# Kernel tuning notes

Measured on AMD Instinct MI355X. Metric: run time of the kernel, lower is better.

The kernel has to match this reference:

```python
import jax, jax.numpy as jnp
import numpy as np

C = 8; E = 512; HEADS = 8; DH = E // HEADS; M = 256; PINV_ITERS = 6; KW = 33

def layer_norm(x, g, b):
    mu = x.mean(-1, keepdims=True)
    xm = x - mu
    v = (xm * xm).mean(-1, keepdims=True)
    return xm / jnp.sqrt(v + 1e-5) * g + b

def mp_pinv(x, iters=PINV_ITERS):
    # Moore-Penrose pseudoinverse via Newton-Schulz iterations (lucidrains nystrom-attention)
    I = jnp.eye(x.shape[-1], dtype=x.dtype)
    ax = jnp.abs(x)
    z = jnp.swapaxes(x, -1, -2) / (jnp.max(ax.sum(-2)) * jnp.max(ax.sum(-1)))
    for _ in range(iters):
        xz = x @ z
        z = 0.25 * z @ (13. * I - xz @ (15. * I - xz @ (7. * I - xz)))
    return z

def nystrom_attn(x, mask, Wqkv, Wout, bout, conv_w):
    b, n0, d = x.shape
    pad = (-n0) % M  # left-pad so seq divisible by num_landmarks
    x = jnp.pad(x, ((0, 0), (pad, 0), (0, 0)))
    mask = jnp.pad(mask, ((0, 0), (pad, 0)))
    n = n0 + pad
    qkv = (x @ Wqkv).reshape(b, n, 3, HEADS, DH).transpose(2, 0, 3, 1, 4)
    q, k, v = qkv[0], qkv[1], qkv[2]  # [b,h,n,dh]
    mf = mask[:, None, :, None].astype(x.dtype)
    q = q * mf * (DH ** -0.5); k = k * mf; v = v * mf
    l = n // M
    mls = mask.reshape(b, 1, M, l).sum(-1).astype(x.dtype)  # valid count per landmark segment
    div = mls[..., None] + 1e-8
    ql = q.reshape(b, HEADS, M, l, DH).sum(3) / div
    kl = k.reshape(b, HEADS, M, l, DH).sum(3) / div
    mland = mls > 0  # [b,1,M]
    neg = -jnp.finfo(x.dtype).max / 2
    sim1 = jnp.where(mask[:, None, :, None] & mland[..., None, :], jnp.einsum('bhid,bhjd->bhij', q, kl), neg)
    sim2 = jnp.where(mland[..., :, None] & mland[..., None, :], jnp.einsum('bhid,bhjd->bhij', ql, kl), neg)
    sim3 = jnp.where(mland[..., :, None] & mask[:, None, None, :], jnp.einsum('bhid,bhjd->bhij', ql, k), neg)
    a1 = jax.nn.softmax(sim1, -1); a2 = jax.nn.softmax(sim2, -1); a3 = jax.nn.softmax(sim3, -1)
    out = (a1 @ mp_pinv(a2)) @ (a3 @ v)
    # residual depthwise conv over sequence dim (residual=True in NystromAttention)
    out = out + jax.lax.conv_general_dilated(v, conv_w, (1, 1), ((KW // 2, KW // 2), (0, 0)),
                                             dimension_numbers=('NCHW', 'OIHW', 'NCHW'),
                                             feature_group_count=HEADS)
    out = out.transpose(0, 2, 1, 3).reshape(b, n, d) @ Wout + bout
    return out[:, pad:]

def _forward(h, W1, b1, cls_token, pmt_token, ln1_g, ln1_b, Wqkv1, Wout1, bout1, conv1,
             ln0_g, ln0_b, Wqkv0, Wout0, bout0, conv0, lnf_g, lnf_b, W3, b3):
    N = h.shape[0]
    h1 = jax.nn.relu(h @ W1 + b1)  # _fc1
    seq = jnp.concatenate([cls_token, pmt_token, h1], 0)[None]  # [1, 1+C+N, E]
    y = nystrom_attn(layer_norm(seq, ln1_g, ln1_b), jnp.ones((1, seq.shape[1]), bool),
                     Wqkv1, Wout1, bout1, conv1)
    x = seq + y  # layer1 (TransLayer_custom)
    pmt = x[:, 1:1 + C, :]   # new pmt tokens [1,C,E]
    toks = x[:, 1 + C:, :]   # [1,N,E]
    assn = jax.nn.softmax(jnp.einsum('bnd,bcd->bnc', toks, pmt), -1)
    idx = jnp.argmax(assn[0], -1)  # [N] cluster assignment
    # cluster dispatch: per-cluster [pmt_i; tokens-of-cluster-i] run of shared layer0, via masking
    xs = jnp.concatenate([pmt[0][:, None, :], jnp.broadcast_to(toks[0], (C, N, E))], 1)  # [C,1+N,E]
    masks = jnp.concatenate([jnp.ones((C, 1), bool), idx[None, :] == jnp.arange(C)[:, None]], 1)
    def trans0(xi, mi):
        xi = xi[None]
        return (xi + nystrom_attn(layer_norm(xi, ln0_g, ln0_b), mi[None], Wqkv0, Wout0, bout0, conv0))[0]
    out = jax.vmap(trans0)(xs, masks)  # [C,1+N,E]
    h_un = out[:, 1:, :][idx, jnp.arange(N)]  # each token from its own cluster's run
    order = jnp.argsort(idx)  # stable: groups tokens by cluster, preserving order (concat order)
    h_global = h_un[order]; idx_new = idx[order]
    hcat = jnp.concatenate([x[0, 0][None], h_global], 0)  # [1+N, E]
    hn = layer_norm(hcat, lnf_g, lnf_b)
    sums = jax.ops.segment_sum(hcat[1:], idx_new, num_segments=C)
    counts = jax.ops.segment_sum(jnp.ones((N,), h.dtype), idx_new, num_segments=C)
    merge = sums / jnp.maximum(counts, 1.)[:, None]  # CTM merge token per cluster
    ptc = jnp.linalg.norm(pmt[0] @ pmt[0].T - jnp.eye(C, dtype=h.dtype))
    tok_out = jnp.concatenate([hn[0][None], merge], 0).mean(0)
    logit = tok_out @ W3 + b3
    return logit, ptc

def setup_inputs() -> dict:
    key = jax.random.key(0)
    ks = jax.random.split(key, 16)
    N, IN_DIM, NC = 4096, 1024, 2
    s = 0.02
    q, _ = jnp.linalg.qr(jax.random.normal(ks[15], (E, C)))  # orthonormal pmt init
    return {
        'h': jax.random.normal(ks[0], (N, IN_DIM)),
        'W1': jax.random.normal(ks[1], (IN_DIM, E)) * s, 'b1': jnp.zeros((E,)),
        'cls_token': jax.random.normal(ks[2], (1, E)),
        'pmt_token': q.T,
        'ln1_g': jnp.ones((E,)), 'ln1_b': jnp.zeros((E,)),
        'Wqkv1': jax.random.normal(ks[3], (E, 3 * E)) * s,
        'Wout1': jax.random.normal(ks[4], (E, E)) * s, 'bout1': jnp.zeros((E,)),
        'conv1': jax.random.normal(ks[5], (HEADS, 1, KW, 1)) * s,
        'ln0_g': jnp.ones((E,)), 'ln0_b': jnp.zeros((E,)),
        'Wqkv0': jax.random.normal(ks[6], (E, 3 * E)) * s,
        'Wout0': jax.random.normal(ks[7], (E, E)) * s, 'bout0': jnp.zeros((E,)),
        'conv0': jax.random.normal(ks[8], (HEADS, 1, KW, 1)) * s,
        'lnf_g': jnp.ones((E,)), 'lnf_b': jnp.zeros((E,)),
        'W3': jax.random.normal(ks[9], (E, NC)) * s, 'b3': jnp.zeros((NC,)),
    }

def reference(h, W1, b1, cls_token, pmt_token, ln1_g, ln1_b, Wqkv1, Wout1, bout1, conv1,
              ln0_g, ln0_b, Wqkv0, Wout0, bout0, conv0, lnf_g, lnf_b, W3, b3):
    logit, ptc = _forward(h, W1, b1, cls_token, pmt_token, ln1_g, ln1_b, Wqkv1, Wout1, bout1, conv1,
                          ln0_g, ln0_b, Wqkv0, Wout0, bout0, conv0, lnf_g, lnf_b, W3, b3)
    return (logit[None], jax.nn.softmax(logit)[None], ptc)
```

## Files before the change

### kernel.cpp

```cpp
#include <hip/hip_runtime.h>

#define NEGV (-1.70141173e38f)

constexpr int E    = 512;
constexpr int NTOK = 4096;
constexpr int NPAD = 4352;
constexpr int PAD1 = 247;
constexpr int NSEQ = 4105;
constexpr int NG   = 5120;
constexpr int NTP  = 4104;

typedef __attribute__((ext_vector_type(8))) short short8;
typedef __attribute__((ext_vector_type(4))) float float4v;

__device__ inline float bf2f(ushort u){ return __uint_as_float(((unsigned)u)<<16); }
__device__ inline ushort f2bf(float f){
  unsigned u = __float_as_uint(f);
  unsigned r = (u + 0x7FFFu + ((u>>16)&1u)) >> 16;
  return (ushort)r;
}
__device__ inline short8 pack8u(const ushort* u) {
  union { short8 v; unsigned w[4]; } x;
  x.w[0] = (unsigned)u[0] | ((unsigned)u[1] << 16);
  x.w[1] = (unsigned)u[2] | ((unsigned)u[3] << 16);
  x.w[2] = (unsigned)u[4] | ((unsigned)u[5] << 16);
  x.w[3] = (unsigned)u[6] | ((unsigned)u[7] << 16);
  return x.v;
}

template<int BT, bool BOUNDS>
__global__ __launch_bounds__(256) void k_mm(
    const ushort* __restrict__ A, const ushort* __restrict__ B,
    const float* __restrict__ bias, const float* __restrict__ resid,
    float* __restrict__ Cf, ushort* __restrict__ Cb,
    int M, int N, int K, int ksplit, int ldC,
    long sA, long sB, long sC,
    const int* __restrict__ colsel, const int* __restrict__ rowsel,
    int zmodA, int zmodB, const int* __restrict__ krange, int kshift,
    float alpha, float bdiag, int flags)
{
  const int z = blockIdx.z;
  const int batch = z / ksplit, ks = z - batch * ksplit;
  const int kslice = K / ksplit;
  int kbeg = ks * kslice, kend = kbeg + kslice;
  if (krange) { int ki = batch >> kshift; kbeg = krange[2*ki]; kend = krange[2*ki+1]; }
  long aoff;
  if (colsel) { int s = colsel[blockIdx.x]; if (s < 0) s = 0; aoff = (long)(s*8 + batch) * sA; }
  else aoff = (long)(zmodA ? (batch & (zmodA-1)) : batch) * sA;
  long boff;
  if (rowsel) { int s = rowsel[blockIdx.y]; if (s < 0) s = 0; boff = (long)(s*8 + batch) * sB; }
  else boff = (long)(zmodB ? (batch & (zmodB-1)) : batch) * sB;
  A += aoff; B += boff;
  const long coff = (long)z * sC;

  __shared__ __align__(16) ushort Al[4][128][8];
  __shared__ __align__(16) ushort Bl[4][128][8];

  const int tid  = threadIdx.x;
  const int lane = tid & 63, wid = tid >> 6;
  const int wr = wid >> 1, wc = wid & 1;
  const int l4 = lane >> 4, l15 = lane & 15;
  const int row0 = blockIdx.y * 128, col0 = blockIdx.x * 128;

  float4v acc[4][4];
#pragma unroll
  for (int i = 0; i < 4; ++i)
#pragma unroll
    for (int j = 0; j < 4; ++j) acc[i][j] = (float4v){0.f,0.f,0.f,0.f};

  for (int k0 = kbeg; k0 < kend; k0 += 32) {
    __syncthreads();
#pragma unroll
    for (int e = 0; e < 2; ++e) {
      int id = tid * 2 + e; int m = id >> 2, kb = id & 3;
      uint4 v = make_uint4(0u,0u,0u,0u);
      int gr = row0 + m;
      if (!BOUNDS || gr < M)
        v = *reinterpret_cast<const uint4*>(A + (long)gr * K + k0 + kb * 8);
      *reinterpret_cast<uint4*>(&Al[kb][m][0]) = v;
    }
    if (BT) {
#pragma unroll
      for (int e = 0; e < 2; ++e) {
        int id = tid * 2 + e; int n = id >> 2, kb = id & 3;
        uint4 v = make_uint4(0u,0u,0u,0u);
        int gc = col0 + n;
        if (!BOUNDS || gc < N)
          v = *reinterpret_cast<const uint4*>(B + (long)gc * K + k0 + kb * 8);
        *reinterpret_cast<uint4*>(&Bl[kb][n][0]) = v;
      }
    } else {
      int n = tid & 127, gc = col0 + n;
      bool inb = (!BOUNDS || gc < N);
#pragma unroll
      for (int e = 0; e < 2; ++e) {
        int kb = (tid >> 7) * 2 + e;
        ushort u[8];
#pragma unroll
        for (int j = 0; j < 8; ++j) {
          int gk = k0 + kb * 8 + j;
          ushort val = inb ? B[(long)gk * N + gc] : (ushort)0;
          if (flags & 4) {
            float f = bdiag * (gk == gc ? 1.f : 0.f) - bf2f(val);
            val = f2bf(f);
          }
          u[j] = val;
        }
        uint4 w;
        w.x = (unsigned)u[0] | ((unsigned)u[1] << 16);
        w.y = (unsigned)u[2] | ((unsigned)u[3] << 16);
        w.z = (unsigned)u[4] | ((unsigned)u[5] << 16);
        w.w = (unsigned)u[6] | ((unsigned)u[7] << 16);
        *reinterpret_cast<uint4*>(&Bl[kb][n][0]) = w;
      }
    }
    __syncthreads();
    short8 af[4], bg[4];
#pragma unroll
    for (int mi = 0; mi < 4; ++mi)
      af[mi] = *reinterpret_cast<const short8*>(&Al[l4][wr*64 + mi*16 + l15][0]);
#pragma unroll
    for (int ni = 0; ni < 4; ++ni)
      bg[ni] = *reinterpret_cast<const short8*>(&Bl[l4][wc*64 + ni*16 + l15][0]);
#pragma unroll
    for (int mi = 0; mi < 4; ++mi)
#pragma unroll
      for (int ni = 0; ni < 4; ++ni)
        acc[mi][ni] = __builtin_amdgcn_mfma_f32_16x16x32_bf16(af[mi], bg[ni], acc[mi][ni], 0, 0, 0);
  }
#pragma unroll
  for (int mi = 0; mi < 4; ++mi)
#pragma unroll
    for (int ni = 0; ni < 4; ++ni)
#pragma unroll
      for (int r = 0; r < 4; ++r) {
        int row = row0 + wr*64 + mi*16 + l4*4 + r;
        int col = col0 + wc*64 + ni*16 + l15;
        if (BOUNDS && (row >= M || col >= N)) continue;
        float v = alpha * acc[mi][ni][r];
        if (flags & 1) v += bias[col];
        if (flags & 2) v = fmaxf(v, 0.f);
        if (flags & 8) v += resid[(long)row * ldC + col];
        long off = coff + (long)row * ldC + col;
        if (flags & 16) Cb[off] = f2bf(v); else Cf[off] = v;
      }
}

static void mm(hipStream_t st, const void* A, const void* B, const float* bias, const float* resid,
               float* Cf, ushort* Cb, int M, int N, int K, int nb, int ksplit, int ldC,
               long sA, long sB, long sC,
               const int* colsel, const int* rowsel, int zmodA, int zmodB,
               const int* krange, int kshift,
               float alpha, float bdiag, int flags, bool bt, bool bounds)
{
  dim3 g((N + 127) / 128, (M + 127) / 128, nb * ksplit), b(256);
  const ushort* a = (const ushort*)A; const ushort* bb = (const ushort*)B;
  if (bt) {
    if (bounds) k_mm<1, true ><<<g, b, 0, st>>>(a, bb, bias, resid, Cf, Cb, M, N, K, ksplit, ldC, sA, sB, sC, colsel, rowsel, zmodA, zmodB, krange, kshift, alpha, bdiag, flags);
    else        k_mm<1, false><<<g, b, 0, st>>>(a, bb, bias, resid, Cf, Cb, M, N, K, ksplit, ldC, sA, sB, sC, colsel, rowsel, zmodA, zmodB, krange, kshift, alpha, bdiag, flags);
  } else {
    if (bounds) k_mm<0, true ><<<g, b, 0, st>>>(a, bb, bias, resid, Cf, Cb, M, N, K, ksplit, ldC, sA, sB, sC, colsel, rowsel, zmodA, zmodB, krange, kshift, alpha, bdiag, flags);
    else        k_mm<0, false><<<g, b, 0, st>>>(a, bb, bias, resid, Cf, Cb, M, N, K, ksplit, ldC, sA, sB, sC, colsel, rowsel, zmodA, zmodB, krange, kshift, alpha, bdiag, flags);
  }
}

__device__ __forceinline__ void gsync() {
  __threadfence();
  __syncthreads();
}

template<int AMODE, int BMODE>
__device__ __forceinline__ void wg_gemm256(
    const ushort* __restrict__ Ag, const ushort* __restrict__ Bg,
    ushort (* __restrict__ Yl)[256], ushort (* __restrict__ Btl)[256],
    float4v acc[8][4], int tid)
{
  const int lane = tid & 63;
  const int wid  = tid >> 6;
  const int wr = wid >> 2, wc = wid & 3;
  const int l4 = lane >> 4, l15 = lane & 15;
#pragma unroll 1
  for (int kt = 0; kt < 8; ++kt) {
    const int k0 = kt * 32;
    if (BMODE == 0) {
      __syncthreads();
      int kk = tid >> 4, n0 = (tid & 15) * 16;
      int s = (kk >> 3) << 4;
      const ushort* src = Bg + (long)(k0 + kk) * 256 + n0;
      *reinterpret_cast<uint4*>(&Btl[kk][n0 ^ s])       = *reinterpret_cast<const uint4*>(src);
      *reinterpret_cast<uint4*>(&Btl[kk][(n0 + 8) ^ s]) = *reinterpret_cast<const uint4*>(src + 8);
      __syncthreads();
    }
    short8 af[8];
#pragma unroll
    for (int mi = 0; mi < 8; ++mi) {
      int r = wr * 128 + mi * 16 + l15;
      if (AMODE == 0) {
        af[mi] = *reinterpret_cast<const short8*>(Ag + (long)r * 256 + k0 + l4 * 8);
      } else {
        int sr = ((r >> 3) & 3) << 4;
        af[mi] = *reinterpret_cast<const short8*>(&Yl[r][(k0 + l4 * 8) ^ sr]);
      }
    }
    short8 bf[4];
#pragma unroll
    for (int ni = 0; ni < 4; ++ni) {
      int c = wc * 64 + ni * 16 + l15;
      ushort u[8];
      if (BMODE == 0) {
        int kb = l4 * 8;
        int cc = c ^ ((kb >> 3) << 4);
#pragma unroll
        for (int j = 0; j < 8; ++j) u[j] = Btl[kb + j][cc];
      } else {
        int kb = k0 + l4 * 8;
        int cc = c ^ (((kb >> 3) & 3) << 4);
#pragma unroll
        for (int j = 0; j < 8; ++j) u[j] = Yl[kb + j][cc];
      }
      bf[ni] = pack8u(u);
    }
#pragma unroll
    for (int mi = 0; mi < 8; ++mi)
#pragma unroll
      for (int ni = 0; ni < 4; ++ni)
        acc[mi][ni] = __builtin_amdgcn_mfma_f32_16x16x32_bf16(af[mi], bf[ni], acc[mi][ni], 0, 0, 0);
  }
}

__global__ __launch_bounds__(512) void k_pinv_chain(
    const ushort* __restrict__ Xall, ushort* __restrict__ ZAall, ushort* __restrict__ ZBall,
    ushort* __restrict__ T1all, ushort* __restrict__ T2all, const float* __restrict__ sc)
{
  __shared__ ushort Yl[256][256];
  __shared__ ushort Btl[32][256];
  const int bt = blockIdx.x;
  const ushort* X = Xall + (long)bt * 65536;
  ushort* Z0 = ZAall + (long)bt * 65536;
  ushort* Z1 = ZBall + (long)bt * 65536;
  ushort* T1 = T1all + (long)bt * 65536;
  ushort* T2 = T2all + (long)bt * 65536;
  const int tid = threadIdx.x;
  const int lane = tid & 63, wid = tid >> 6;
  const int wr = wid >> 2, wc = wid & 3;
  const int l4 = lane >> 4, l15 = lane & 15;
  const float scale = sc[bt >> 3];

  {
    int r = tid & 255, half = tid >> 8;
    for (int c0 = half * 128; c0 < half * 128 + 128; c0 += 8) {
      ushort u[8];
#pragma unroll
      for (int j = 0; j < 8; ++j)
        u[j] = f2bf(bf2f(X[(long)(c0 + j) * 256 + r]) * scale);
      *reinterpret_cast<short8*>(Z0 + (long)r * 256 + c0) = pack8u(u);
    }
  }
  gsync();

  ushort* Zc = Z0;
  ushort* Zn = Z1;
  float4v acc[8][4];

  for (int it = 0; it < 6; ++it) {
#pragma unroll
    for (int i = 0; i < 8; ++i)
#pragma unroll
      for (int j = 0; j < 4; ++j) acc[i][j] = (float4v){0.f,0.f,0.f,0.f};
    wg_gemm256<0,0>(X, Zc, Yl, Btl, acc, tid);
    __syncthreads();
#pragma unroll
    for (int mi = 0; mi < 8; ++mi)
#pragma unroll
      for (int ni = 0; ni < 4; ++ni)
#pragma unroll
        for (int ri = 0; ri < 4; ++ri) {
          int row = wr*128 + mi*16 + l4*4 + ri;
          int col = wc*64 + ni*16 + l15;
          Yl[row][col ^ (((row >> 3) & 3) << 4)] = f2bf(acc[mi][ni][ri]);
        }
    __syncthreads();
#pragma unroll
    for (int i = 0; i < 8; ++i)
#pragma unroll
      for (int j = 0; j < 4; ++j) acc[i][j] = (float4v){0.f,0.f,0.f,0.f};
    wg_gemm256<1,1>(nullptr, nullptr, Yl, Btl, acc, tid);
#pragma unroll
    for (int mi = 0; mi < 8; ++mi)
#pragma unroll
      for (int ni = 0; ni < 4; ++ni)
#pragma unroll
        for (int ri = 0; ri < 4; ++ri) {
          int row = wr*128 + mi*16 + l4*4 + ri;
          int col = wc*64 + ni*16 + l15;
          float y = bf2f(Yl[row][col ^ (((row >> 3) & 3) << 4)]);
          T1[(long)row*256 + col] = f2bf(7.f*y - acc[mi][ni][ri]);
        }
    gsync();
#pragma unroll
    for (int i = 0; i < 8; ++i)
#pragma unroll
      for (int j = 0; j < 4; ++j) acc[i][j] = (float4v){0.f,0.f,0.f,0.f};
    wg_gemm256<1,0>(nullptr, T1, Yl, Btl, acc, tid);
#pragma unroll
    for (int mi = 0; mi < 8; ++mi)
#pragma unroll
      for (int ni = 0; ni < 4; ++ni)
#pragma unroll
        for (int ri = 0; ri < 4; ++ri) {
          int row = wr*128 + mi*16 + l4*4 + ri;
          int col = wc*64 + ni*16 + l15;
          float y = bf2f(Yl[row][col ^ (((row >> 3) & 3) << 4)]);
          T2[(long)row*256 + col] = f2bf(15.f*y - acc[mi][ni][ri]);
        }
    gsync();
#pragma unroll
    for (int i = 0; i < 8; ++i)
#pragma unroll
      for (int j = 0; j < 4; ++j) acc[i][j] = (float4v){0.f,0.f,0.f,0.f};
    wg_gemm256<0,0>(Zc, T2, Yl, Btl, acc, tid);
#pragma unroll
    for (int mi = 0; mi < 8; ++mi)
#pragma unroll
      for (int ni = 0; ni < 4; ++ni)
#pragma unroll
        for (int ri = 0; ri < 4; ++ri) {
          int row = wr*128 + mi*16 + l4*4 + ri;
          int col = wc*64 + ni*16 + l15;
          float zv = bf2f(Zc[(long)row*256 + col]);
          Zn[(long)row*256 + col] = f2bf(0.25f*(13.f*zv - acc[mi][ni][ri]));
        }
    gsync();
    ushort* tmp = Zc; Zc = Zn; Zn = tmp;
  }
}

__global__ __launch_bounds__(256) void k_colmax(const ushort* __restrict__ X, float* __restrict__ sc) {
  int cl = blockIdx.x, j = threadIdx.x;
  float cmax = 0.f;
  for (int h = 0; h < 8; ++h) {
    const ushort* mat = X + (long)(cl * 8 + h) * 65536;
    float cs = 0.f;
    for (int i = 0; i < 256; ++i) cs += bf2f(mat[i * 256 + j]);
    cmax = fmaxf(cmax, cs);
  }
  __shared__ float red[256];
  red[j] = cmax; __syncthreads();
  for (int o = 128; o > 0; o >>= 1) { if (j < o) red[j] = fmaxf(red[j], red[j + o]); __syncthreads(); }
  if (j == 0) sc[cl] = 1.f / red[0];
}

__global__ void k_prep0(const float* __restrict__ cls, const float* __restrict__ pmt, float* __restrict__ seq) {
  int i = blockIdx.x * 256 + threadIdx.x;
  if (i < 512) seq[i] = cls[i];
  else if (i < 4608) seq[i] = pmt[i - 512];
}
__global__ void k_cvt(const float* __restrict__ s, ushort* __restrict__ d, long n) {
  long i = (long)blockIdx.x * 256 + threadIdx.x;
  if (i < n) d[i] = f2bf(s[i]);
}
__global__ void k_tcvt_all(const float* __restrict__ W1, const float* __restrict__ Wq1,
                           const float* __restrict__ Wq0, const float* __restrict__ Wo1,
                           const float* __restrict__ Wo0,
                           ushort* __restrict__ W1t, ushort* __restrict__ Wq1t,
                           ushort* __restrict__ Wq0t, ushort* __restrict__ Wo1t,
                           ushort* __restrict__ Wo0t) {
  const float* W; ushort* Wt; int K, N;
  switch (blockIdx.z) {
    case 0:  W = W1;  Wt = W1t;  K = 1024; N = 512;  break;
    case 1:  W = Wq1; Wt = Wq1t; K = 512;  N = 1536; break;
    case 2:  W = Wq0; Wt = Wq0t; K = 512;  N = 1536; break;
    case 3:  W = Wo1; Wt = Wo1t; K = 512;  N = 512;  break;
    default: W = Wo0; Wt = Wo0t; K = 512;  N = 512;  break;
  }
  int nb_ = blockIdx.x * 32, kb = blockIdx.y * 32;
  if (nb_ >= N || kb >= K) return;
  __shared__ float tile[32][33];
  int tx = threadIdx.x, ty = threadIdx.y;
  for (int r = ty; r < 32; r += 8) tile[r][tx] = W[(long)(kb + r) * N + nb_ + tx];
  __syncthreads();
  for (int r = ty; r < 32; r += 8) Wt[(long)(nb_ + r) * K + kb + tx] = f2bf(tile[tx][r]);
}

__device__ __forceinline__ void ln_row(const float* __restrict__ xr, const float* __restrict__ g,
                                       const float* __restrict__ b, ushort* __restrict__ yr,
                                       float* red, int t) {
  float v0 = xr[t], v1 = xr[t + 256];
  red[t] = v0 + v1; __syncthreads();
  for (int o = 128; o > 0; o >>= 1) { if (t < o) red[t] += red[t + o]; __syncthreads(); }
  float mu = red[0] * (1.f / E); __syncthreads();
  float d0 = v0 - mu, d1 = v1 - mu;
  red[t] = d0 * d0 + d1 * d1; __syncthreads();
  for (int o = 128; o > 0; o >>= 1) { if (t < o) red[t] += red[t + o]; __syncthreads(); }
  float inv = 1.f / sqrtf(red[0] * (1.f / E) + 1e-5f);
  yr[t]       = f2bf(d0 * inv * g[t]       + b[t]);
  yr[t + 256] = f2bf(d1 * inv * g[t + 256] + b[t + 256]);
}

__global__ __launch_bounds__(256) void k_lnB(const float* __restrict__ x, const float* __restrict__ g,
                                             const float* __restrict__ b, ushort* __restrict__ y) {
  int row = blockIdx.x, t = threadIdx.x;
  ushort* yr = y + (long)row * E;
  if (row < PAD1) { yr[t] = 0; yr[t + 256] = 0; return; }
  __shared__ float red[256];
  ln_row(x + (long)(row - PAD1) * E, g, b, yr, red, t);
}
__global__ __launch_bounds__(256) void k_lnC(const float* __restrict__ seq, const float* __restrict__ g,
                                             const float* __restrict__ b, ushort* __restrict__ y) {
  int row = blockIdx.x, t = threadIdx.x;
  const float* xr = (row < 8) ? (seq + 512 + (long)row * E) : (seq + 9 * 512 + (long)(row - 8) * E);
  __shared__ float red[256];
  ln_row(xr, g, b, y + (long)row * E, red, t);
}

__global__ void k_buildQKVB(const float* __restrict__ qkv, ushort* __restrict__ Qb,
                            ushort* __restrict__ Kb, ushort* __restrict__ Vt) {
  int h = blockIdx.y, p0 = blockIdx.x * 64;
  int tx = threadIdx.x & 63, tg = threadIdx.x >> 6;
  __shared__ float tile[64][65];
  for (int r = tg; r < 64; r += 4) {
    long src = (long)(p0 + r) * 1536 + h * 64 + tx;
    long o = ((long)h * NPAD + p0 + r) * 64 + tx;
    Qb[o] = f2bf(qkv[src]);
    Kb[o] = f2bf(qkv[src + 512]);
    tile[r][tx] = qkv[src + 1024];
  }
  __syncthreads();
  for (int d = tg; d < 64; d += 4) Vt[((long)h * 64 + d) * NPAD + p0 + tx] = f2bf(tile[tx][d]);
}
__global__ void k_gatherQKV(const float* __restrict__ qkvall, const int* __restrict__ gtok,
                            ushort* __restrict__ Qg, ushort* __restrict__ Kg, ushort* __restrict__ Vgt) {
  int h = blockIdx.y, p0 = blockIdx.x * 64;
  int tx = threadIdx.x & 63, tg = threadIdx.x >> 6;
  __shared__ float tile[64][65];
  for (int r = tg; r < 64; r += 4) {
    int tk = gtok[p0 + r];
    int srcrow = tk >= 0 ? 8 + tk : (tk <= -2 ? (-2 - tk) : -1);
    float q = 0.f, k = 0.f, v = 0.f;
    if (srcrow >= 0) {
      long s = (long)srcrow * 1536 + h * 64 + tx;
      q = qkvall[s]; k = qkvall[s + 512]; v = qkvall[s + 1024];
    }
    long o = ((long)h * NG + p0 + r) * 64 + tx;
    Qg[o] = f2bf(q); Kg[o] = f2bf(k);
    tile[r][tx] = v;
  }
  __syncthreads();
  for (int d = tg; d < 64; d += 4) Vgt[((long)h * 64 + d) * NG + p0 + tx] = f2bf(tile[tx][d]);
}

__global__ void k_qlkl_B(const float* __restrict__ qkv, ushort* __restrict__ ql, ushort* __restrict__ kl,
                         float* __restrict__ mlandB) {
  int i = blockIdx.x, h = blockIdx.y, d = threadIdx.x;
  float sq = 0.f, sk = 0.f; int cnt = 0;
  for (int j = 0; j < 17; ++j) {
    int p = i * 17 + j;
    if (p >= PAD1) {
      sq += qkv[(long)p * 1536 + h * 64 + d];
      sk += qkv[(long)p * 1536 + 512 + h * 64 + d];
      cnt++;
    }
  }
  float dv = (float)cnt + 1e-8f;
  ql[((long)h * 256 + i) * 64 + d] = f2bf(sq * 0.125f / dv);
  kl[((long)h * 256 + i) * 64 + d] = f2bf(sk / dv);
  if (h == 0 && d == 0) mlandB[i] = cnt > 0 ? 1.f : 0.f;
}

__global__ void k_qlkl_C(const float* __restrict__ qkvall, const int* __restrict__ idx,
                         ushort* __restrict__ qlc, ushort* __restrict__ klc,
                         float* __restrict__ mland_c) {
  int i = blockIdx.x, bt = blockIdx.y;
  int c = bt >> 3, h = bt & 7, d = threadIdx.x;
  float sq = 0.f, sk = 0.f; int cnt = 0;
  for (int j = 0; j < 17; ++j) {
    int p = i * 17 + j;
    int srcrow = -1;
    if (p == 255) srcrow = c;
    else if (p >= 256 && idx[p - 256] == c) srcrow = 8 + (p - 256);
    if (srcrow >= 0) {
      const float* src = qkvall + (long)srcrow * 1536 + h * 64;
      sq += src[d]; sk += src[512 + d];
      cnt++;
    }
  }
  float dv = (float)cnt + 1e-8f;
  qlc[((long)bt * 256 + i) * 64 + d] = f2bf(sq * 0.125f / dv);
  klc[((long)bt * 256 + i) * 64 + d] = f2bf(sk / dv);
  if (h == 0 && d == 0) mland_c[c * 256 + i] = cnt > 0 ? 1.f : 0.f;
}

__global__ __launch_bounds__(256) void k_a2soft(const float* __restrict__ S2, const float* __restrict__ mland,
                                                ushort* __restrict__ X) {
  int i = blockIdx.x, bt = blockIdx.y, j = threadIdx.x;
  int cl = bt >> 3;
  const float* Sr = S2 + ((long)bt * 256 + i) * 256;
  __shared__ float red[256];
  float landi = mland[cl * 256 + i];
  float out;
  if (landi > 0.f) {
    bool valid = mland[cl * 256 + j] > 0.f;
    float sv = valid ? Sr[j] : NEGV;
    red[j] = sv; __syncthreads();
    for (int o = 128; o > 0; o >>= 1) { if (j < o) red[j] = fmaxf(red[j], red[j + o]); __syncthreads(); }
    float mx = red[0]; __syncthreads();
    float e = valid ? expf(sv - mx) : 0.f;
    red[j] = e; __syncthreads();
    for (int o = 128; o > 0; o >>= 1) { if (j < o) red[j] += red[j + o]; __syncthreads(); }
    out = e / red[0];
  } else {
    out = 1.f / 256.f;
  }
  X[((long)bt * 256 + i) * 256 + j] = f2bf(out);
}

__global__ __launch_bounds__(256) void k_smaxB_av(const float* __restrict__ S, ushort* __restrict__ P,
                                                  const float* __restrict__ mland) {
  int i = blockIdx.x, h = blockIdx.y, t = threadIdx.x;
  const float* Sr = S + ((long)h * 256 + i) * NPAD;
  ushort* Pr = P + ((long)h * 256 + i) * NPAD;
  __shared__ float sv[NPAD];
  __shared__ float red[256];
  if (mland[i] > 0.f) {
    float lmax = NEGV;
    for (int j = t; j < NPAD; j += 256) {
      float s = Sr[j];
      sv[j] = s;
      if (j >= PAD1) lmax = fmaxf(lmax, s);
    }
    red[t] = lmax; __syncthreads();
    for (int o = 128; o > 0; o >>= 1) { if (t < o) red[t] = fmaxf(red[t], red[t + o]); __syncthreads(); }
    float mx = red[0]; __syncthreads();
    float lsum = 0.f;
    for (int j = t; j < NPAD; j += 256) {
      float e = (j >= PAD1) ? expf(sv[j] - mx) : 0.f;
      sv[j] = e; lsum += e;
    }
    red[t] = lsum; __syncthreads();
    for (int o = 128; o > 0; o >>= 1) { if (t < o) red[t] += red[t + o]; __syncthreads(); }
    float inv = 1.f / red[0];
    for (int j = t; j < NPAD; j += 256) Pr[j] = f2bf(sv[j] * inv);
  } else {
    const float u = 1.f / 4352.f;
    for (int j = t; j < NPAD; j += 256) Pr[j] = f2bf(j >= PAD1 ? u : 0.f);
  }
}

__global__ __launch_bounds__(256) void k_smaxseg(const float* __restrict__ S3, ushort* __restrict__ P3,
                                                 const float* __restrict__ mlandC, const int* __restrict__ gclu,
                                                 const int* __restrict__ segb) {
  int i = blockIdx.x, bt = blockIdx.y, t = threadIdx.x;
  int c = bt >> 3, h = bt & 7;
  const float* Sr = S3 + ((long)h * 256 + i) * NG;
  ushort* Pr = P3 + ((long)h * 256 + i) * NG;
  int jb = segb[c], je = segb[c + 1];
  __shared__ float sv[4352];
  __shared__ float red[256];
  if (mlandC[c * 256 + i] > 0.f) {
    float lmax = NEGV;
    for (int j = jb + t; j < je; j += 256) {
      float s = Sr[j];
      sv[j - jb] = s;
      if (gclu[j] == c) lmax = fmaxf(lmax, s);
    }
    red[t] = lmax; __syncthreads();
    for (int o = 128; o > 0; o >>= 1) { if (t < o) red[t] = fmaxf(red[t], red[t + o]); __syncthreads(); }
    float mx = red[0]; __syncthreads();
    float lsum = 0.f;
    for (int j = jb + t; j < je; j += 256) {
      float e = (gclu[j] == c) ? expf(sv[j - jb] - mx) : 0.f;
      sv[j - jb] = e; lsum += e;
    }
    red[t] = lsum; __syncthreads();
    for (int o = 128; o > 0; o >>= 1) { if (t < o) red[t] += red[t + o]; __syncthreads(); }
    float inv = 1.f / red[0];
    for (int j = jb + t; j < je; j += 256) Pr[j] = f2bf(sv[j - jb] * inv);
  } else {
    const float u = 1.f / 4352.f;
    for (int j = jb + t; j < je; j += 256) Pr[j] = f2bf(gclu[j] == c ? u : 0.f);
  }
}

template<int MODE>
__global__ __launch_bounds__(256) void k_smax256(const float* __restrict__ S, ushort* __restrict__ P,
                                                 const float* __restrict__ mland, const int* __restrict__ gtok,
                                                 const int* __restrict__ gclu, int rows) {
  int row = blockIdx.x, h = blockIdx.y, j = threadIdx.x;
  const float* Sr = S + ((long)h * rows + row) * 256;
  ushort* Pr = P + ((long)h * rows + row) * 256;
  int c = 0;
  if (MODE == 1) {
    int tk = gtok[row];
    if (tk < 0) { Pr[j] = 0; return; }
    c = gclu[row];
  }
  bool mem = (MODE == 1) ? (mland[c * 256 + j] > 0.f) : (mland[j] > 0.f);
  __shared__ float red[256];
  float s = mem ? Sr[j] : NEGV;
  red[j] = s; __syncthreads();
  for (int o = 128; o > 0; o >>= 1) { if (j < o) red[j] = fmaxf(red[j], red[j + o]); __syncthreads(); }
  float mx = red[0]; __syncthreads();
  float e = mem ? expf(s - mx) : 0.f;
  red[j] = e; __syncthreads();
  for (int o = 128; o > 0; o >>= 1) { if (j < o) red[j] += red[j + o]; __syncthreads(); }
  Pr[j] = f2bf(e / red[0]);
}

__global__ void k_avredB(const float* __restrict__ sl, ushort* __restrict__ avb, int ks) {
  int i = blockIdx.x, h = blockIdx.y, d = threadIdx.x;
  float s = 0.f;
  for (int k = 0; k < ks; ++k) s += sl[(((long)h * ks + k) * 256 + i) * 64 + d];
  avb[((long)h * 256 + i) * 64 + d] = f2bf(s);
}

__global__ void k_conv_B(const float* __restrict__ qkv, const float* __restrict__ w,
                         const float* __restrict__ preout, ushort* __restrict__ lnb) {
  int r = blockIdx.x, t = threadIdx.x;
  int h = t >> 6;
  int prow = PAD1 + r;
  float acc = preout[(long)prow * E + t];
  for (int tt = 0; tt < 33; ++tt) {
    int p = prow + tt - 16;
    if (p < NPAD) acc += qkv[(long)p * 1536 + 1024 + t] * w[h * 33 + tt];
  }
  lnb[(long)r * E + t] = f2bf(acc);
}

__global__ void k_idxptc(const float* __restrict__ x, int* __restrict__ idx, float* __restrict__ ptc_out) {
  int t = threadIdx.x;
  __shared__ float red[64];
  if (blockIdx.x == NTOK) {
    int a = t >> 3, b = t & 7;
    const float* pmt = x + E;
    float s = 0.f;
    for (int d = 0; d < E; ++d) s += pmt[(long)a * E + d] * pmt[(long)b * E + d];
    s -= (a == b) ? 1.f : 0.f;
    red[t] = s * s; __syncthreads();
    for (int o = 32; o > 0; o >>= 1) { if (t < o) red[t] += red[t + o]; __syncthreads(); }
    if (t == 0) *ptc_out = sqrtf(red[0]);
    return;
  }
  int n = blockIdx.x;
  const float* tok = x + (long)(9 + n) * E;
  const float* pmt = x + E;
  int c = t >> 3, part = t & 7;
  float s = 0.f;
  for (int d = part * 64; d < part * 64 + 64; ++d) s += tok[d] * pmt[(long)c * E + d];
  red[t] = s; __syncthreads();
  if (t < 8) {
    float dot = 0.f;
    for (int p = 0; p < 8; ++p) dot += red[t * 8 + p];
    red[t] = dot;
  }
  __syncthreads();
  if (t == 0) {
    int best = 0; float bv = red[0];
    for (int c2 = 1; c2 < 8; ++c2) if (red[c2] > bv) { bv = red[c2]; best = c2; }
    idx[n] = best;
  }
}

__global__ __launch_bounds__(256) void k_gprep(const int* __restrict__ idx, int* __restrict__ gtok,
                                               int* __restrict__ gclu, int* __restrict__ gpos,
                                               int* __restrict__ segb, int* __restrict__ krange,
                                               int* __restrict__ blkclu) {
  __shared__ int hist[8][16];
  __shared__ int boff[8][16];
  __shared__ int segs[9];
  __shared__ int sidx[256];
  int t = threadIdx.x;
  if (t < 128) ((int*)hist)[t] = 0;
  __syncthreads();
  for (int b = 0; b < 16; ++b) atomicAdd(&hist[idx[b * 256 + t]][b], 1);
  __syncthreads();
  if (t == 0) {
    int s = 0;
    for (int c = 0; c < 8; ++c) {
      segs[c] = s;
      int run = s + 1, tot = 1;
      for (int b = 0; b < 16; ++b) { boff[c][b] = run; run += hist[c][b]; tot += hist[c][b]; }
      krange[2 * c] = s;
      krange[2 * c + 1] = s + ((tot + 31) & ~31);
      s += (tot + 127) & ~127;
    }
    segs[8] = s;
    for (int c = 0; c <= 8; ++c) segb[c] = segs[c];
  }
  __syncthreads();
  for (int g = t; g < NG; g += 256) { gtok[g] = -1; gclu[g] = -1; }
  __syncthreads();
  if (t < 8) { gtok[segs[t]] = -2 - t; gclu[segs[t]] = t; }
  for (int b = t; b < NG / 128; b += 256) {
    int cl = -1;
    for (int c = 0; c < 8; ++c) if (b * 128 >= segs[c] && b * 128 < segs[c + 1]) cl = c;
    blkclu[b] = cl;
  }
  for (int b = 0; b < 16; ++b) {
    int n = b * 256 + t;
    int c = idx[n];
    sidx[t] = c;
    __syncthreads();
    int rank = 0;
    for (int m = 0; m < t; ++m) rank += (sidx[m] == c);
    int pos = boff[c][b] + rank;
    gtok[pos] = n; gclu[pos] = c; gpos[n] = pos;
    __syncthreads();
  }
}

__global__ void k_outC(const float* __restrict__ OUTg, const int* __restrict__ gpos,
                       const int* __restrict__ idx, const float* __restrict__ qkvall,
                       const float* __restrict__ w, ushort* __restrict__ lnb) {
  int n = blockIdx.x, t = threadIdx.x;
  int h = t >> 6;
  int c = idx[n];
  float acc = OUTg[(long)gpos[n] * 512 + t];
  for (int tt = 0; tt < 33; ++tt) {
    int m = n + tt - 16;
    float vv = 0.f;
    if (m == -1) vv = qkvall[(long)c * 1536 + 1024 + t];
    else if (m >= 0 && m < NTOK && idx[m] == c) vv = qkvall[(long)(8 + m) * 1536 + 1024 + t];
    acc += vv * w[h * 33 + tt];
  }
  lnb[(long)n * E + t] = f2bf(acc);
}

__global__ void k_seg_part(const float* __restrict__ hun, const int* __restrict__ idx,
                           float* __restrict__ part, float* __restrict__ pcnt) {
  int c = blockIdx.x, sl = blockIdx.y, d = threadIdx.x;
  float s = 0.f; int cnt = 0;
  for (int n = sl * 256; n < sl * 256 + 256; ++n) {
    if (idx[n] == c) { s += hun[(long)n * E + d]; if (d == 0) cnt++; }
  }
  part[(long)(c * 16 + sl) * E + d] = s;
  if (d == 0) pcnt[c * 16 + sl] = (float)cnt;
}

__global__ void k_final(const float* __restrict__ x0, const float* __restrict__ g, const float* __restrict__ b,
                        const float* __restrict__ part, const float* __restrict__ pcnt,
                        const float* __restrict__ ptc, const float* __restrict__ W3, const float* __restrict__ b3,
                        float* __restrict__ out) {
  int t = threadIdx.x;
  __shared__ float red[512];
  float xv = x0[t];
  red[t] = xv; __syncthreads();
  for (int o = 256; o > 0; o >>= 1) { if (t < o) red[t] += red[t + o]; __syncthreads(); }
  float mu = red[0] * (1.f / 512.f); __syncthreads();
  float d0 = xv - mu;
  red[t] = d0 * d0; __syncthreads();
  for (int o = 256; o > 0; o >>= 1) { if (t < o) red[t] += red[t + o]; __syncthreads(); }
  float inv = 1.f / sqrtf(red[0] * (1.f / 512.f) + 1e-5f);
  __syncthreads();
  float acc = d0 * inv * g[t] + b[t];
  for (int c = 0; c < 8; ++c) {
    float s = 0.f, cnt = 0.f;
    for (int sl = 0; sl < 16; ++sl) { s += part[(long)(c * 16 + sl) * E + t]; cnt += pcnt[c * 16 + sl]; }
    acc += s / fmaxf(cnt, 1.f);
  }
  float tk = acc * (1.f / 9.f);
  red[t] = tk * W3[t * 2 + 0]; __syncthreads();
  for (int o = 256; o > 0; o >>= 1) { if (t < o) red[t] += red[t + o]; __syncthreads(); }
  float l0 = red[0] + b3[0]; __syncthreads();
  red[t] = tk * W3[t * 2 + 1]; __syncthreads();
  for (int o = 256; o > 0; o >>= 1) { if (t < o) red[t] += red[t + o]; __syncthreads(); }
  float l1 = red[0] + b3[1];
  if (t == 0) {
    out[0] = l0; out[1] = l1;
    float mx = fmaxf(l0, l1);
    float e0 = expf(l0 - mx), e1 = expf(l1 - mx), s = e0 + e1;
    out[2] = e0 / s; out[3] = e1 / s;
    out[4] = *ptc;
  }
}

extern "C" void kernel_launch(void* const* d_in, const int* in_sizes, int n_in,
                              void* d_out, int out_size, void* d_ws, size_t ws_size,
                              hipStream_t stream) {
  const float* h_in  = (const float*)d_in[0];
  const float* W1    = (const float*)d_in[1];
  const float* b1    = (const float*)d_in[2];
  const float* cls   = (const float*)d_in[3];
  const float* pmt_t = (const float*)d_in[4];
  const float* ln1_g = (const float*)d_in[5];
  const float* ln1_b = (const float*)d_in[6];
  const float* Wqkv1 = (const float*)d_in[7];
  const float* Wout1 = (const float*)d_in[8];
  const float* bout1 = (const float*)d_in[9];
  const float* conv1 = (const float*)d_in[10];
  const float* ln0_g = (const float*)d_in[11];
  const float* ln0_b = (const float*)d_in[12];
  const float* Wqkv0 = (const float*)d_in[13];
  const float* Wout0 = (const float*)d_in[14];
  const float* bout0 = (const float*)d_in[15];
  const float* conv0 = (const float*)d_in[16];
  const float* lnf_g = (const float*)d_in[17];
  const float* lnf_b = (const float*)d_in[18];
  const float* W3    = (const float*)d_in[19];
  const float* b3    = (const float*)d_in[20];

  char* base = (char*)d_ws;
  size_t off = 0;
  auto alloc = [&](size_t b) -> void* {
    off = (off + 255) & ~(size_t)255;
    void* p = base + off; off += b; return p;
  };
  float*  SEQ    = (float*) alloc((size_t)NSEQ * E * 4);
  float*  QKV    = (float*) alloc((size_t)NPAD * 1536 * 4);
  ushort* W1t    = (ushort*)alloc((size_t)512 * 1024 * 2);
  ushort* Wq1t   = (ushort*)alloc((size_t)1536 * 512 * 2);
  ushort* Wq0t   = (ushort*)alloc((size_t)1536 * 512 * 2);
  ushort* Wo1t   = (ushort*)alloc((size_t)512 * 512 * 2);
  ushort* Wo0t   = (ushort*)alloc((size_t)512 * 512 * 2);
  ushort* LNb    = (ushort*)alloc((size_t)NPAD * E * 2);
  ushort* QbU    = (ushort*)alloc((size_t)8 * NG * 64 * 2);
  ushort* KbU    = (ushort*)alloc((size_t)8 * NG * 64 * 2);
  ushort* VtU    = (ushort*)alloc((size_t)8 * NG * 64 * 2);
  char*   U1     = (char*)  alloc((size_t)8 * 256 * NG * 4);
  char*   U2     = (char*)  alloc((size_t)8 * 256 * NG * 2);
  ushort* PXb    = (ushort*)alloc((size_t)64 * 65536 * 2);
  ushort* PZa    = (ushort*)alloc((size_t)64 * 65536 * 2);
  ushort* qlbB   = (ushort*)alloc((size_t)8 * 16384 * 2);
  ushort* klbB   = (ushort*)alloc((size_t)8 * 16384 * 2);
  ushort* qlcb   = (ushort*)alloc((size_t)64 * 16384 * 2);
  ushort* klcb   = (ushort*)alloc((size_t)64 * 16384 * 2);
  float*  avsl   = (float*) alloc((size_t)8 * 8 * 16384 * 4);
  ushort* avb    = (ushort*)alloc((size_t)64 * 16384 * 2);
  ushort* Wcb    = (ushort*)alloc((size_t)64 * 16384 * 2);
  float*  PREOUT = (float*) alloc((size_t)NPAD * E * 4);
  float*  mlandB = (float*) alloc(256 * 4);
  float*  mlandC = (float*) alloc(8 * 256 * 4);
  int*    idx    = (int*)   alloc(NTOK * 4);
  int*    gtok   = (int*)   alloc(NG * 4);
  int*    gclu   = (int*)   alloc(NG * 4);
  int*    gpos   = (int*)   alloc(NTOK * 4);
  int*    segb   = (int*)   alloc(9 * 4);
  int*    krange = (int*)   alloc(16 * 4);
  int*    blkclu = (int*)   alloc((NG / 128) * 4);
  float*  ptc    = (float*) alloc(256);
  float*  sc     = (float*) alloc(256);
  float*  part   = (float*) alloc((size_t)8 * 16 * 512 * 4);
  float*  pcnt   = (float*) alloc(8 * 16 * 4);

  ushort* hb   = (ushort*)U1;
  float*  Sbuf = (float*)U1;
  ushort* ZBc  = (ushort*)U1;
  ushort* T1c  = (ushort*)(U1 + (size_t)64 * 65536 * 2);
  ushort* T2c  = (ushort*)(U1 + (size_t)2 * 64 * 65536 * 2);
  float*  OUTg = (float*)U1;
  ushort* Pbuf = (ushort*)U2;

  k_tcvt_all<<<dim3(48, 32, 5), dim3(32, 8), 0, stream>>>(W1, Wqkv1, Wqkv0, Wout1, Wout0,
                                                          W1t, Wq1t, Wq0t, Wo1t, Wo0t);
  k_prep0<<<dim3(18), dim3(256), 0, stream>>>(cls, pmt_t, SEQ);
  k_cvt<<<dim3(16384), dim3(256), 0, stream>>>(h_in, hb, (long)4096 * 1024);
  mm(stream, hb, W1t, b1, nullptr, SEQ + 9 * 512, nullptr, 4096, 512, 1024, 1, 1, 512,
     0, 0, 0, nullptr, nullptr, 0, 0, nullptr, 0, 1.f, 0.f, 1 | 2, true, false);

  k_lnB<<<dim3(NPAD), dim3(256), 0, stream>>>(SEQ, ln1_g, ln1_b, LNb);
  mm(stream, LNb, Wq1t, nullptr, nullptr, QKV, nullptr, NPAD, 1536, 512, 1, 1, 1536,
     0, 0, 0, nullptr, nullptr, 0, 0, nullptr, 0, 1.f, 0.f, 0, true, false);
  k_buildQKVB<<<dim3(NPAD / 64, 8), dim3(256), 0, stream>>>(QKV, QbU, KbU, VtU);
  k_qlkl_B<<<dim3(256, 8), dim3(64), 0, stream>>>(QKV, qlbB, klbB, mlandB);
  mm(stream, qlbB, klbB, nullptr, nullptr, Sbuf, nullptr, 256, 256, 64, 8, 1, 256,
     16384, 16384, 65536, nullptr, nullptr, 0, 0, nullptr, 0, 1.f, 0.f, 0, true, false);
  k_a2soft<<<dim3(256, 8), dim3(256), 0, stream>>>(Sbuf, mlandB, PXb);
  k_colmax<<<dim3(1), dim3(256), 0, stream>>>(PXb, sc);
  k_pinv_chain<<<dim3(8), dim3(512), 0, stream>>>(PXb, PZa, ZBc, T1c, T2c, sc);
  mm(stream, qlbB, KbU, nullptr, nullptr, Sbuf, nullptr, 256, NPAD, 64, 8, 1, NPAD,
     16384, (long)NPAD * 64, (long)256 * NPAD, nullptr, nullptr, 0, 0, nullptr, 0, 1.f, 0.f, 0, true, false);
  k_smaxB_av<<<dim3(256, 8), dim3(256), 0, stream>>>(Sbuf, Pbuf, mlandB);
  mm(stream, Pbuf, VtU, nullptr, nullptr, avsl, nullptr, 256, 64, NPAD, 8, 8, 64,
     (long)256 * NPAD, (long)64 * NPAD, 16384, nullptr, nullptr, 0, 0, nullptr, 0, 1.f, 0.f, 0, true, true);
  k_avredB<<<dim3(256, 8), dim3(64), 0, stream>>>(avsl, avb, 8);
  mm(stream, PZa, avb, nullptr, nullptr, nullptr, Wcb, 256, 64, 256, 8, 1, 64,
     65536, 16384, 16384, nullptr, nullptr, 0, 0, nullptr, 0, 1.f, 0.f, 16, false, true);
  mm(stream, QbU + PAD1 * 64, klbB, nullptr, nullptr, Sbuf, nullptr, NSEQ, 256, 64, 8, 1, 256,
     (long)NPAD * 64, 16384, (long)NSEQ * 256, nullptr, nullptr, 0, 0, nullptr, 0, 0.125f, 0.f, 0, true, true);
  k_smax256<0><<<dim3(NSEQ, 8), dim3(256), 0, stream>>>(Sbuf, Pbuf, mlandB, nullptr, nullptr, NSEQ);
  mm(stream, Pbuf, Wcb, nullptr, nullptr, PREOUT + (long)PAD1 * 512, nullptr, NSEQ, 64, 256, 8, 1, 512,
     (long)NSEQ * 256, 16384, 64, nullptr, nullptr, 0, 0, nullptr, 0, 1.f, 0.f, 0, false, true);
  k_conv_B<<<dim3(NSEQ), dim3(512), 0, stream>>>(QKV, conv1, PREOUT, LNb);
  mm(stream, LNb, Wo1t, bout1, SEQ, SEQ, nullptr, NSEQ, 512, 512, 1, 1, 512,
     0, 0, 0, nullptr, nullptr, 0, 0, nullptr, 0, 1.f, 0.f, 1 | 8, true, true);

  k_idxptc<<<dim3(NTOK + 1), dim3(64), 0, stream>>>(SEQ, idx, ptc);
  k_gprep<<<dim3(1), dim3(256), 0, stream>>>(idx, gtok, gclu, gpos, segb, krange, blkclu);
  k_lnC<<<dim3(NTP), dim3(256), 0, stream>>>(SEQ, ln0_g, ln0_b, LNb);
  mm(stream, LNb, Wq0t, nullptr, nullptr, QKV, nullptr, NTP, 1536, 512, 1, 1, 1536,
     0, 0, 0, nullptr, nullptr, 0, 0, nullptr, 0, 1.f, 0.f, 0, true, true);
  k_qlkl_C<<<dim3(256, 64), dim3(64), 0, stream>>>(QKV, idx, qlcb, klcb, mlandC);
  k_gatherQKV<<<dim3(NG / 64, 8), dim3(256), 0, stream>>>(QKV, gtok, QbU, KbU, VtU);
  mm(stream, qlcb, klcb, nullptr, nullptr, Sbuf, nullptr, 256, 256, 64, 64, 1, 256,
     16384, 16384, 65536, nullptr, nullptr, 0, 0, nullptr, 0, 1.f, 0.f, 0, true, false);
  k_a2soft<<<dim3(256, 64), dim3(256), 0, stream>>>(Sbuf, mlandC, PXb);
  k_colmax<<<dim3(8), dim3(256), 0, stream>>>(PXb, sc);
  k_pinv_chain<<<dim3(64), dim3(512), 0, stream>>>(PXb, PZa, ZBc, T1c, T2c, sc);
  mm(stream, qlcb, KbU, nullptr, nullptr, Sbuf, nullptr, 256, NG, 64, 8, 1, NG,
     16384, (long)NG * 64, (long)256 * NG, blkclu, nullptr, 0, 0, nullptr, 0, 1.f, 0.f, 0, true, false);
  k_smaxseg<<<dim3(256, 64), dim3(256), 0, stream>>>(Sbuf, Pbuf, mlandC, gclu, segb);
  mm(stream, Pbuf, VtU, nullptr, nullptr, nullptr, avb, 256, 64, NG, 64, 1, 64,
     (long)256 * NG, (long)64 * NG, 16384, nullptr, nullptr, 8, 8, krange, 3, 1.f, 0.f, 16, true, true);
  mm(stream, PZa, avb, nullptr, nullptr, nullptr, Wcb, 256, 64, 256, 64, 1, 64,
     65536, 16384, 16384, nullptr, nullptr, 0, 0, nullptr, 0, 1.f, 0.f, 16, false, true);
  mm(stream, QbU, klcb, nullptr, nullptr, Sbuf, nullptr, NG, 256, 64, 8, 1, 256,
     (long)NG * 64, 16384, (long)NG * 256, nullptr, blkclu, 0, 0, nullptr, 0, 0.125f, 0.f, 0, true, false);
  k_smax256<1><<<dim3(NG, 8), dim3(256), 0, stream>>>(Sbuf, Pbuf, mlandC, gtok, gclu, NG);
  mm(stream, Pbuf, Wcb, nullptr, nullptr, OUTg, nullptr, NG, 64, 256, 8, 1, 512,
     (long)NG * 256, 16384, 64, nullptr, blkclu, 0, 0, nullptr, 0, 1.f, 0.f, 0, false, true);
  k_outC<<<dim3(NTOK), dim3(512), 0, stream>>>(OUTg, gpos, idx, QKV, conv0, LNb);
  mm(stream, LNb, Wo0t, bout0, SEQ + 9 * 512, PREOUT, nullptr, NTOK, 512, 512, 1, 1, 512,
     0, 0, 0, nullptr, nullptr, 0, 0, nullptr, 0, 1.f, 0.f, 1 | 8, true, false);

  k_seg_part<<<dim3(8, 16), dim3(512), 0, stream>>>(PREOUT, idx, part, pcnt);
  k_final<<<dim3(1), dim3(512), 0, stream>>>(SEQ, lnf_g, lnf_b, part, pcnt, ptc, W3, b3,
                                             (float*)d_out);
}
```

Before: 2.513 ms.

## Split fused per-matrix pinv kernel into batched tiled GEMM launches

Replaces the persistent `k_pinv_chain` kernel, which ran one 512-thread workgroup per 256x256 matrix, with a new transpose-scale kernel for Z0 (`k_z0`) plus four generic batched `mm` launches per Newton-Schulz iteration. The per-iteration scalar-times-identity and diagonal terms are pushed into the GEMM epilogue via the bdiag/alpha flags. The goal is to spread the work over many more workgroups (128x128 tiles per matrix), since the fused version launched only 8 or 64 blocks on a large GPU. In exchange it adds 24 kernel launches per pseudoinverse and round-trips intermediates through global memory instead of LDS.

```diff
diff --git a/kernel.cpp b/kernel.cpp
--- a/kernel.cpp
+++ b/kernel.cpp
@@ -18,14 +18,6 @@
   unsigned u = __float_as_uint(f);
   unsigned r = (u + 0x7FFFu + ((u>>16)&1u)) >> 16;
   return (ushort)r;
-}
-__device__ inline short8 pack8u(const ushort* u) {
-  union { short8 v; unsigned w[4]; } x;
-  x.w[0] = (unsigned)u[0] | ((unsigned)u[1] << 16);
-  x.w[1] = (unsigned)u[2] | ((unsigned)u[3] << 16);
-  x.w[2] = (unsigned)u[4] | ((unsigned)u[5] << 16);
-  x.w[3] = (unsigned)u[6] | ((unsigned)u[7] << 16);
-  return x.v;
 }
 
 template<int BT, bool BOUNDS>
@@ -164,175 +156,22 @@
   }
 }
 
-__device__ __forceinline__ void gsync() {
-  __threadfence();
-  __syncthreads();
-}
-
-template<int AMODE, int BMODE>
-__device__ __forceinline__ void wg_gemm256(
-    const ushort* __restrict__ Ag, const ushort* __restrict__ Bg,
-    ushort (* __restrict__ Yl)[256], ushort (* __restrict__ Btl)[256],
-    float4v acc[8][4], int tid)
-{
-  const int lane = tid & 63;
-  const int wid  = tid >> 6;
-  const int wr = wid >> 2, wc = wid & 3;
-  const int l4 = lane >> 4, l15 = lane & 15;
-#pragma unroll 1
-  for (int kt = 0; kt < 8; ++kt) {
-    const int k0 = kt * 32;
-    if (BMODE == 0) {
-      __syncthreads();
-      int kk = tid >> 4, n0 = (tid & 15) * 16;
-      int s = (kk >> 3) << 4;
-      const ushort* src = Bg + (long)(k0 + kk) * 256 + n0;
-      *reinterpret_cast<uint4*>(&Btl[kk][n0 ^ s])       = *reinterpret_cast<const uint4*>(src);
-      *reinterpret_cast<uint4*>(&Btl[kk][(n0 + 8) ^ s]) = *reinterpret_cast<const uint4*>(src + 8);
-      __syncthreads();
-    }
-    short8 af[8];
-#pragma unroll
-    for (int mi = 0; mi < 8; ++mi) {
-      int r = wr * 128 + mi * 16 + l15;
-      if (AMODE == 0) {
-        af[mi] = *reinterpret_cast<const short8*>(Ag + (long)r * 256 + k0 + l4 * 8);
-      } else {
-        int sr = ((r >> 3) & 3) << 4;
-        af[mi] = *reinterpret_cast<const short8*>(&Yl[r][(k0 + l4 * 8) ^ sr]);
-      }
-    }
-    short8 bf[4];
-#pragma unroll
-    for (int ni = 0; ni < 4; ++ni) {
-      int c = wc * 64 + ni * 16 + l15;
-      ushort u[8];
-      if (BMODE == 0) {
-        int kb = l4 * 8;
-        int cc = c ^ ((kb >> 3) << 4);
-#pragma unroll
-        for (int j = 0; j < 8; ++j) u[j] = Btl[kb + j][cc];
-      } else {
-        int kb = k0 + l4 * 8;
-        int cc = c ^ (((kb >> 3) & 3) << 4);
-#pragma unroll
-        for (int j = 0; j < 8; ++j) u[j] = Yl[kb + j][cc];
-      }
-      bf[ni] = pack8u(u);
-    }
-#pragma unroll
-    for (int mi = 0; mi < 8; ++mi)
-#pragma unroll
-      for (int ni = 0; ni < 4; ++ni)
-        acc[mi][ni] = __builtin_amdgcn_mfma_f32_16x16x32_bf16(af[mi], bf[ni], acc[mi][ni], 0, 0, 0);
-  }
-}
-
-__global__ __launch_bounds__(512) void k_pinv_chain(
-    const ushort* __restrict__ Xall, ushort* __restrict__ ZAall, ushort* __restrict__ ZBall,
-    ushort* __restrict__ T1all, ushort* __restrict__ T2all, const float* __restrict__ sc)
-{
-  __shared__ ushort Yl[256][256];
-  __shared__ ushort Btl[32][256];
-  const int bt = blockIdx.x;
-  const ushort* X = Xall + (long)bt * 65536;
-  ushort* Z0 = ZAall + (long)bt * 65536;
-  ushort* Z1 = ZBall + (long)bt * 65536;
-  ushort* T1 = T1all + (long)bt * 65536;
-  ushort* T2 = T2all + (long)bt * 65536;
-  const int tid = threadIdx.x;
-  const int lane = tid & 63, wid = tid >> 6;
-  const int wr = wid >> 2, wc = wid & 3;
-  const int l4 = lane >> 4, l15 = lane & 15;
-  const float scale = sc[bt >> 3];
-
-  {
-    int r = tid & 255, half = tid >> 8;
-    for (int c0 = half * 128; c0 < half * 128 + 128; c0 += 8) {
-      ushort u[8];
-#pragma unroll
-      for (int j = 0; j < 8; ++j)
-        u[j] = f2bf(bf2f(X[(long)(c0 + j) * 256 + r]) * scale);
-      *reinterpret_cast<short8*>(Z0 + (long)r * 256 + c0) = pack8u(u);
-    }
-  }
-  gsync();
-
-  ushort* Zc = Z0;
-  ushort* Zn = Z1;
-  float4v acc[8][4];
-
+static void pinv_iters(hipStream_t st, const ushort* PX, ushort* PZ, ushort* Y, ushort* T1, ushort* T2, int nb) {
+  ushort* z = PZ; ushort* y = Y;
   for (int it = 0; it < 6; ++it) {
-#pragma unroll
-    for (int i = 0; i < 8; ++i)
-#pragma unroll
-      for (int j = 0; j < 4; ++j) acc[i][j] = (float4v){0.f,0.f,0.f,0.f};
-    wg_gemm256<0,0>(X, Zc, Yl, Btl, acc, tid);
-    __syncthreads();
-#pragma unroll
-    for (int mi = 0; mi < 8; ++mi)
-#pragma unroll
-      for (int ni = 0; ni < 4; ++ni)
-#pragma unroll
-        for (int ri = 0; ri < 4; ++ri) {
-          int row = wr*128 + mi*16 + l4*4 + ri;
-          int col = wc*64 + ni*16 + l15;
-          Yl[row][col ^ (((row >> 3) & 3) << 4)] = f2bf(acc[mi][ni][ri]);
-        }
-    __syncthreads();
-#pragma unroll
-    for (int i = 0; i < 8; ++i)
-#pragma unroll
-      for (int j = 0; j < 4; ++j) acc[i][j] = (float4v){0.f,0.f,0.f,0.f};
-    wg_gemm256<1,1>(nullptr, nullptr, Yl, Btl, acc, tid);
-#pragma unroll
-    for (int mi = 0; mi < 8; ++mi)
-#pragma unroll
-      for (int ni = 0; ni < 4; ++ni)
-#pragma unroll
-        for (int ri = 0; ri < 4; ++ri) {
-          int row = wr*128 + mi*16 + l4*4 + ri;
-          int col = wc*64 + ni*16 + l15;
-          float y = bf2f(Yl[row][col ^ (((row >> 3) & 3) << 4)]);
-          T1[(long)row*256 + col] = f2bf(7.f*y - acc[mi][ni][ri]);
-        }
-    gsync();
-#pragma unroll
-    for (int i = 0; i < 8; ++i)
-#pragma unroll
-      for (int j = 0; j < 4; ++j) acc[i][j] = (float4v){0.f,0.f,0.f,0.f};
-    wg_gemm256<1,0>(nullptr, T1, Yl, Btl, acc, tid);
-#pragma unroll
-    for (int mi = 0; mi < 8; ++mi)
-#pragma unroll
-      for (int ni = 0; ni < 4; ++ni)
-#pragma unroll
-        for (int ri = 0; ri < 4; ++ri) {
-          int row = wr*128 + mi*16 + l4*4 + ri;
-          int col = wc*64 + ni*16 + l15;
-          float y = bf2f(Yl[row][col ^ (((row >> 3) & 3) << 4)]);
-          T2[(long)row*256 + col] = f2bf(15.f*y - acc[mi][ni][ri]);
-        }
-    gsync();
-#pragma unroll
-    for (int i = 0; i < 8; ++i)
-#pragma unroll
-      for (int j = 0; j < 4; ++j) acc[i][j] = (float4v){0.f,0.f,0.f,0.f};
-    wg_gemm256<0,0>(Zc, T2, Yl, Btl, acc, tid);
-#pragma unroll
-    for (int mi = 0; mi < 8; ++mi)
-#pragma unroll
-      for (int ni = 0; ni < 4; ++ni)
-#pragma unroll
-        for (int ri = 0; ri < 4; ++ri) {
-          int row = wr*128 + mi*16 + l4*4 + ri;
-          int col = wc*64 + ni*16 + l15;
-          float zv = bf2f(Zc[(long)row*256 + col]);
-          Zn[(long)row*256 + col] = f2bf(0.25f*(13.f*zv - acc[mi][ni][ri]));
-        }
-    gsync();
-    ushort* tmp = Zc; Zc = Zn; Zn = tmp;
-  }
+    mm(st, PX, z,  nullptr, nullptr, nullptr, y,  256,256,256, nb,1,256, 65536,65536,65536, nullptr,nullptr,0,0,nullptr,0, 1.f,   0.f, 16,    false, false);
+    mm(st, y,  y,  nullptr, nullptr, nullptr, T1, 256,256,256, nb,1,256, 65536,65536,65536, nullptr,nullptr,0,0,nullptr,0, 1.f,   7.f, 16|4,  false, false);
+    mm(st, y,  T1, nullptr, nullptr, nullptr, T2, 256,256,256, nb,1,256, 65536,65536,65536, nullptr,nullptr,0,0,nullptr,0, 1.f,  15.f, 16|4,  false, false);
+    mm(st, z,  T2, nullptr, nullptr, nullptr, y,  256,256,256, nb,1,256, 65536,65536,65536, nullptr,nullptr,0,0,nullptr,0, 0.25f,13.f, 16|4,  false, false);
+    ushort* tmp = z; z = y; y = tmp;
+  }
+}
+
+__global__ void k_z0(const ushort* __restrict__ X, const float* __restrict__ sc, ushort* __restrict__ Z, int nb) {
+  long t = (long)blockIdx.x * 256 + threadIdx.x;
+  if (t >= (long)nb * 65536) return;
+  int bt = (int)(t >> 16); int ij = (int)(t & 65535); int i = ij >> 8, j = ij & 255;
+  Z[t] = f2bf(bf2f(X[((long)bt << 16) + j * 256 + i]) * sc[bt >> 3]);
 }
 
 __global__ __launch_bounds__(256) void k_colmax(const ushort* __restrict__ X, float* __restrict__ sc) {
@@ -843,7 +682,7 @@
 
   ushort* hb   = (ushort*)U1;
   float*  Sbuf = (float*)U1;
-  ushort* ZBc  = (ushort*)U1;
+  ushort* Ybuf = (ushort*)U1;
   ushort* T1c  = (ushort*)(U1 + (size_t)64 * 65536 * 2);
   ushort* T2c  = (ushort*)(U1 + (size_t)2 * 64 * 65536 * 2);
   float*  OUTg = (float*)U1;
@@ -865,7 +704,8 @@
      16384, 16384, 65536, nullptr, nullptr, 0, 0, nullptr, 0, 1.f, 0.f, 0, true, false);
   k_a2soft<<<dim3(256, 8), dim3(256), 0, stream>>>(Sbuf, mlandB, PXb);
   k_colmax<<<dim3(1), dim3(256), 0, stream>>>(PXb, sc);
-  k_pinv_chain<<<dim3(8), dim3(512), 0, stream>>>(PXb, PZa, ZBc, T1c, T2c, sc);
+  k_z0<<<dim3((8 * 65536) / 256), dim3(256), 0, stream>>>(PXb, sc, PZa, 8);
+  pinv_iters(stream, PXb, PZa, Ybuf, T1c, T2c, 8);
   mm(stream, qlbB, KbU, nullptr, nullptr, Sbuf, nullptr, 256, NPAD, 64, 8, 1, NPAD,
      16384, (long)NPAD * 64, (long)256 * NPAD, nullptr, nullptr, 0, 0, nullptr, 0, 1.f, 0.f, 0, true, false);
   k_smaxB_av<<<dim3(256, 8), dim3(256), 0, stream>>>(Sbuf, Pbuf, mlandB);
@@ -894,7 +734,8 @@
      16384, 16384, 65536, nullptr, nullptr, 0, 0, nullptr, 0, 1.f, 0.f, 0, true, false);
   k_a2soft<<<dim3(256, 64), dim3(256), 0, stream>>>(Sbuf, mlandC, PXb);
   k_colmax<<<dim3(8), dim3(256), 0, stream>>>(PXb, sc);
-  k_pinv_chain<<<dim3(64), dim3(512), 0, stream>>>(PXb, PZa, ZBc, T1c, T2c, sc);
+  k_z0<<<dim3((64 * 65536) / 256), dim3(256), 0, stream>>>(PXb, sc, PZa, 64);
+  pinv_iters(stream, PXb, PZa, Ybuf, T1c, T2c, 64);
   mm(stream, qlcb, KbU, nullptr, nullptr, Sbuf, nullptr, 256, NG, 64, 8, 1, NG,
      16384, (long)NG * 64, (long)256 * NG, blkclu, nullptr, 0, 0, nullptr, 0, 1.f, 0.f, 0, true, false);
   k_smaxseg<<<dim3(256, 64), dim3(256), 0, stream>>>(Sbuf, Pbuf, mlandC, gclu, segb);
```

Measured after the change: 2.612 ms. +3.9%, slower.
